# Performance work log

Hardware: AMD Instinct MI355X
Metric: run time of the kernel (lower is better)

Reference implementation:

```python
import jax, jax.numpy as jnp
import numpy as np

EPS = 1e-5
BN_GAMMA = 1.0
BN_BETA = 1e-4  # per torch init: BN weight=1, bias=0.0001


def bn(h):
    # BatchNorm1d in training mode: biased batch variance
    mu = h.mean(axis=0)
    var = h.var(axis=0)
    return (h - mu) * (BN_GAMMA / jnp.sqrt(var + EPS)) + BN_BETA


def gcn_conv(h, W, b, row, col, n, edge_weight=None):
    # PyG-style GCNConv: linear -> add self loops (w=1) -> sym deg norm -> scatter-sum
    h = h @ W
    e = row.shape[0]
    ew = jnp.ones((e,), h.dtype) if edge_weight is None else edge_weight
    loop = jnp.arange(n, dtype=row.dtype)
    r = jnp.concatenate([row, loop])
    c = jnp.concatenate([col, loop])
    w = jnp.concatenate([ew, jnp.ones((n,), h.dtype)])
    deg = jax.ops.segment_sum(w, r, num_segments=n)
    dinv = jnp.where(deg > 0, jax.lax.rsqrt(deg + jnp.where(deg > 0, 0.0, 1.0)), 0.0)
    norm = dinv[r] * w * dinv[c]  # [E+N]
    msg = h[r] * norm[:, None]    # gather + per-edge scale
    out = jax.ops.segment_sum(msg, c, num_segments=n)  # scatter-aggregate
    return out + b


def readout(h, W1, b1, W2, b2):
    h = bn(h) @ W1 + b1
    h = bn(jax.nn.relu(h)) @ W2 + b2
    return jax.nn.log_softmax(h, axis=-1)


def setup_inputs() -> dict:
    key = jax.random.key(0)
    ks = jax.random.split(key, 12)
    N, E, F, H, C = 50000, 800000, 128, 128, 10
    s = 0.05
    return {
        "x": jax.random.normal(ks[0], (N, F), jnp.float32),
        "edge_index": jax.random.randint(ks[1], (2, E), 0, N, jnp.int32),
        "perm": jax.random.permutation(ks[2], N).astype(jnp.int32),
        "W_feat": jax.random.normal(ks[3], (F, H), jnp.float32) * s,
        "b_feat": jnp.zeros((H,), jnp.float32),
        "W_convs": jax.random.normal(ks[4], (3, H, H), jnp.float32) * s,
        "b_convs": jnp.zeros((3, H), jnp.float32),
        "W_ea": jax.random.normal(ks[5], (2 * H, 2), jnp.float32) * s,
        "b_ea": jnp.zeros((2,), jnp.float32),
        "W_na": jax.random.normal(ks[6], (H, 2), jnp.float32) * s,
        "b_na": jnp.zeros((2,), jnp.float32),
        "W_ctx": jax.random.normal(ks[7], (H, H), jnp.float32) * s,
        "b_ctx": jnp.zeros((H,), jnp.float32),
        "W_obj": jax.random.normal(ks[8], (H, H), jnp.float32) * s,
        "b_obj": jnp.zeros((H,), jnp.float32),
        "W_fc1": jax.random.normal(ks[9], (3, H, H), jnp.float32) * s,  # c,o,co
        "b_fc1": jnp.zeros((3, H), jnp.float32),
        "W_fc2": jax.random.normal(ks[10], (3, H, C), jnp.float32) * s,
        "b_fc2": jnp.zeros((3, C), jnp.float32),
    }


def reference(x, edge_index, perm, W_feat, b_feat, W_convs, b_convs, W_ea, b_ea,
              W_na, b_na, W_ctx, b_ctx, W_obj, b_obj, W_fc1, b_fc1, W_fc2, b_fc2):
    n = x.shape[0]
    row, col = edge_index[0], edge_index[1]
    h = bn(x)
    h = jax.nn.relu(h @ W_feat + b_feat)  # conv_feat has gfn=True -> pure linear
    for i in range(3):
        h = jax.nn.relu(gcn_conv(bn(h), W_convs[i], b_convs[i], row, col, n))
    edge_rep = jnp.concatenate([h[row], h[col]], axis=-1)  # [E, 2H]
    edge_att = jax.nn.softmax(edge_rep @ W_ea + b_ea, axis=-1)
    node_att = jax.nn.softmax(h @ W_na + b_na, axis=-1)
    xc = node_att[:, 0:1] * h
    xo = node_att[:, 1:2] * h
    xc = jax.nn.relu(gcn_conv(bn(xc), W_ctx, b_ctx, row, col, n, edge_att[:, 0]))
    xo = jax.nn.relu(gcn_conv(bn(xo), W_obj, b_obj, row, col, n, edge_att[:, 1]))
    xc_logis = readout(xc, W_fc1[0], b_fc1[0], W_fc2[0], b_fc2[0])
    xo_logis = readout(xo, W_fc1[1], b_fc1[1], W_fc2[1], b_fc2[1])
    xco_logis = readout(xc[perm] + xo, W_fc1[2], b_fc1[2], W_fc2[2], b_fc2[2])
    return (xc_logis, xo_logis, xco_logis)
```

## Files before the change

### kernel.cpp

```cpp
#include <hip/hip_runtime.h>
#include <math.h>

#define H 128
#define NCLS 10
#define EPS 1e-5f
#define BN_BETA 1e-4f
#define CS_BLOCKS 256

typedef unsigned short u16;
typedef unsigned int u32;
typedef __attribute__((ext_vector_type(8))) short short8;
typedef __attribute__((ext_vector_type(4))) float floatx4;

__device__ inline float bflo(u32 u) { union { u32 i; float f; } a; a.i = u << 16; return a.f; }
__device__ inline float bfhi(u32 u) { union { u32 i; float f; } a; a.i = u & 0xffff0000u; return a.f; }
__device__ inline u16 f2bf(float f) {
  union { float f; u32 i; } v; v.f = f;
  return (u16)((v.i + 0x7fff + ((v.i >> 16) & 1)) >> 16);
}
__device__ inline u32 pack2(float a, float b) { return (u32)f2bf(a) | ((u32)f2bf(b) << 16); }

__device__ inline void reduce_partials(const float* __restrict__ P, int nb, int stride,
                                       int off0, int f, float* su_out, float* sq_out) {
  float su[8] = {0, 0, 0, 0, 0, 0, 0, 0}, sq[8] = {0, 0, 0, 0, 0, 0, 0, 0};
  int b = 0;
  for (; b + 8 <= nb; b += 8) {
#pragma unroll
    for (int u = 0; u < 8; u++) {
      const float* p = P + (size_t)(b + u) * stride + off0;
      su[u] += p[f];
      sq[u] += p[128 + f];
    }
  }
  for (; b < nb; b++) {
    const float* p = P + (size_t)b * stride + off0;
    su[0] += p[f];
    sq[0] += p[128 + f];
  }
  *su_out = ((su[0] + su[1]) + (su[2] + su[3])) + ((su[4] + su[5]) + (su[6] + su[7]));
  *sq_out = ((sq[0] + sq[1]) + (sq[2] + sq[3])) + ((sq[4] + sq[5]) + (sq[6] + sq[7]));
}

__device__ inline void fold256_body(const float* P, int nb, int stride, int off0,
                                    const float* W, const float* bias, float invN,
                                    int kp, u16* Wt, float* cf) {
  int f = threadIdx.x & 127;
  int half = threadIdx.x >> 7;
  int k = kp * 2 + half;
  float su, sq;
  reduce_partials(P, nb, stride, off0, f, &su, &sq);
  float mu = su * invN;
  float var = sq * invN - mu * mu;
  float s = 1.0f / sqrtf(fmaxf(var, 0.f) + EPS);
  float w = W[(size_t)f * H + k];
  Wt[(size_t)k * H + f] = f2bf(s * w);
  __shared__ float red[2][128];
  red[half][f] = (BN_BETA - mu * s) * w;
  __syncthreads();
  for (int o = 64; o > 0; o >>= 1) {
    if (f < o) red[half][f] += red[half][f + o];
    __syncthreads();
  }
  if (f == 0) cf[k] = red[half][0] + (bias ? bias[k] : 0.f);
}

__device__ inline void hist_body(const int* __restrict__ row, const int* __restrict__ col,
                                 int E, int* cnt_in, int* cnt_out,
                                 int* rank_in, int* rank_out, int blk) {
  int e = blk * 256 + threadIdx.x;
  if (e < E) {
    rank_in[e] = atomicAdd(&cnt_in[col[e]], 1);
    rank_out[e] = atomicAdd(&cnt_out[row[e]], 1);
  }
}

__device__ inline void xstats_body(const float* __restrict__ x, int n4,
                                   float* __restrict__ stp, int blk) {
  int tid = threadIdx.x;
  int lane = tid & 63, wave = tid >> 6;
  float s[4] = {0, 0, 0, 0}, q[4] = {0, 0, 0, 0};
  int step = CS_BLOCKS * 256;
  for (int i = blk * 256 + tid; i < n4; i += step) {
    float4 v = ((const float4*)x)[i];
    s[0] += v.x; q[0] += v.x * v.x; s[1] += v.y; q[1] += v.y * v.y;
    s[2] += v.z; q[2] += v.z * v.z; s[3] += v.w; q[3] += v.w * v.w;
  }
#pragma unroll
  for (int k = 0; k < 4; k++) { s[k] += __shfl_xor(s[k], 32); q[k] += __shfl_xor(q[k], 32); }
  __shared__ float smx[4][256];
  int col = (lane & 31) * 4;
  if (lane < 32) {
#pragma unroll
    for (int k = 0; k < 4; k++) { smx[wave][col + k] = s[k]; smx[wave][128 + col + k] = q[k]; }
  }
  __syncthreads();
  stp[(size_t)blk * 256 + tid] = smx[0][tid] + smx[1][tid] + smx[2][tid] + smx[3][tid];
}

__device__ inline void scanA_body(const int* cnt_in, const int* cnt_out, int N,
                                  int* partial_in, int* partial_out, float* dinv, int blk) {
  int i = blk * 256 + threadIdx.x;
  int vo = (i < N) ? cnt_out[i] : 0;
  if (i < N) dinv[i] = 1.0f / sqrtf((float)vo + 1.0f);
  __shared__ int sdA[256];
  sdA[threadIdx.x] = (i < N) ? cnt_in[i] : 0;
  __syncthreads();
  for (int o = 128; o > 0; o >>= 1) {
    if (threadIdx.x < o) sdA[threadIdx.x] += sdA[threadIdx.x + o];
    __syncthreads();
  }
  if (threadIdx.x == 0) partial_in[blk] = sdA[0];
  __syncthreads();
  sdA[threadIdx.x] = vo;
  __syncthreads();
  for (int o = 128; o > 0; o >>= 1) {
    if (threadIdx.x < o) sdA[threadIdx.x] += sdA[threadIdx.x + o];
    __syncthreads();
  }
  if (threadIdx.x == 0) partial_out[blk] = sdA[0];
}

__device__ inline void scanB1(const int* partial, int nb, int* blockoff) {
  __shared__ int sdB[256];
  int t = threadIdx.x;
  int v = (t < nb) ? partial[t] : 0;
  sdB[t] = v;
  __syncthreads();
  for (int o = 1; o < 256; o <<= 1) {
    int x = (t >= o) ? sdB[t - o] : 0;
    __syncthreads();
    sdB[t] += x;
    __syncthreads();
  }
  blockoff[t] = sdB[t] - v;
  __syncthreads();
}

__device__ inline void scanC1(const int* cnt, int N, const int* blockoff,
                              int* off, int E, int blk) {
  __shared__ int sdC[256];
  int t = threadIdx.x;
  int i = blk * 256 + t;
  int v = (i < N) ? cnt[i] : 0;
  sdC[t] = v;
  __syncthreads();
  for (int o = 1; o < 256; o <<= 1) {
    int x = (t >= o) ? sdC[t - o] : 0;
    __syncthreads();
    sdC[t] += x;
    __syncthreads();
  }
  if (i < N) off[i] = blockoff[blk] + sdC[t] - v;
  if (i == 0) off[N] = E;
  __syncthreads();
}

__device__ inline void place_body(const int* row, const int* col, int E,
                                  const int* rank_in, const int* rank_out,
                                  const int* off_in, const int* off_out,
                                  const float* dinv, int* csr_src, int* slot_in,
                                  int* sout, float* wn, int blk) {
  int e = blk * 256 + threadIdx.x;
  if (e < E) {
    int c = col[e], r = row[e];
    int si = off_in[c] + rank_in[e];
    csr_src[si] = r;
    slot_in[e] = si;
    wn[si] = dinv[r];
    sout[e] = off_out[r] + rank_out[e];
  }
}

__device__ inline void eatt_body(const int* row, const int* col, int E,
                                 const float2* p01, const float2* q01,
                                 const float* b_ea, const int* slot_in,
                                 const int* sout, float* att0s, float* att_r, int blk) {
  int e = blk * 256 + threadIdx.x;
  if (e >= E) return;
  int r = row[e], c = col[e];
  float2 p = p01[r], q = q01[c];
  float l0 = p.x + q.x + b_ea[0];
  float l1 = p.y + q.y + b_ea[1];
  float a0 = 1.0f / (1.0f + expf(l1 - l0));
  att0s[slot_in[e]] = a0;
  att_r[sout[e]] = a0;
}

__device__ inline void degsum_body(const float* att_r, const int* off_out,
                                   float* degc, int N, int blk) {
  int v = blk * 256 + threadIdx.x;
  if (v >= N) return;
  int s0 = off_out[v], s1 = off_out[v + 1];
  float s = 0.f;
  for (int i = s0; i < s1; i++) s += att_r[i];
  degc[v] = s;
}

__device__ inline void xprestats_body(const u16* __restrict__ h,
                                      const float2* __restrict__ na01, int n4,
                                      float* __restrict__ stp, int blk) {
  int tid = threadIdx.x;
  int lane = tid & 63, wave = tid >> 6;
  float sc[4] = {0, 0, 0, 0}, qc[4] = {0, 0, 0, 0};
  float so[4] = {0, 0, 0, 0}, qo[4] = {0, 0, 0, 0};
  int step = CS_BLOCKS * 256;
  for (int i = blk * 256 + tid; i < n4; i += step) {
    int n = i >> 5;
    uint2 u = ((const uint2*)h)[i];
    float v0 = bflo(u.x), v1 = bfhi(u.x), v2 = bflo(u.y), v3 = bfhi(u.y);
    float2 ab = na01[n];
    float a = ab.x, b = ab.y;
    float c0 = v0 * a, c1 = v1 * a, c2 = v2 * a, c3 = v3 * a;
    float o0 = v0 * b, o1 = v1 * b, o2 = v2 * b, o3 = v3 * b;
    sc[0] += c0; qc[0] += c0 * c0; sc[1] += c1; qc[1] += c1 * c1;
    sc[2] += c2; qc[2] += c2 * c2; sc[3] += c3; qc[3] += c3 * c3;
    so[0] += o0; qo[0] += o0 * o0; so[1] += o1; qo[1] += o1 * o1;
    so[2] += o2; qo[2] += o2 * o2; so[3] += o3; qo[3] += o3 * o3;
  }
#pragma unroll
  for (int k = 0; k < 4; k++) {
    sc[k] += __shfl_xor(sc[k], 32); qc[k] += __shfl_xor(qc[k], 32);
    so[k] += __shfl_xor(so[k], 32); qo[k] += __shfl_xor(qo[k], 32);
  }
  __shared__ float smp[4][512];
  int col = (lane & 31) * 4;
  if (lane < 32) {
#pragma unroll
    for (int k = 0; k < 4; k++) {
      smp[wave][col + k] = sc[k];
      smp[wave][128 + col + k] = qc[k];
      smp[wave][256 + col + k] = so[k];
      smp[wave][384 + col + k] = qo[k];
    }
  }
  __syncthreads();
  float r0 = smp[0][tid] + smp[1][tid] + smp[2][tid] + smp[3][tid];
  float r1 = smp[0][256 + tid] + smp[1][256 + tid] + smp[2][256 + tid] + smp[3][256 + tid];
  stp[(size_t)blk * 512 + tid] = r0;
  stp[(size_t)blk * 512 + 256 + tid] = r1;
}

__device__ inline void gemm_core(const u16* A, const float* Afp, const u16* Bt,
                                 const float* cf, const float* b2, const float* sumw,
                                 u16* C, int N, int relu, int blk, float* stp) {
  int tid = threadIdx.x;
  int wave = tid >> 6, lane = tid & 63;
  int l15 = lane & 15, quad = lane >> 4;
  int row0 = (blk * 4 + wave) * 16;
  if (row0 >= N && !stp) return;
  int arow = row0 + l15;
  short8 a[4];
  short8 z8 = {0, 0, 0, 0, 0, 0, 0, 0};
  if (Afp) {
#pragma unroll
    for (int k4 = 0; k4 < 4; k4++) {
      if (arow < N) {
        const float* p = Afp + (size_t)arow * H + k4 * 32 + quad * 8;
        float4 f0 = *(const float4*)p;
        float4 f1 = *(const float4*)(p + 4);
        union { short8 s8; u32 u[4]; } cv;
        cv.u[0] = pack2(f0.x, f0.y); cv.u[1] = pack2(f0.z, f0.w);
        cv.u[2] = pack2(f1.x, f1.y); cv.u[3] = pack2(f1.z, f1.w);
        a[k4] = cv.s8;
      } else a[k4] = z8;
    }
  } else {
#pragma unroll
    for (int k4 = 0; k4 < 4; k4++)
      a[k4] = (arow < N) ? *(const short8*)(A + (size_t)arow * H + k4 * 32 + quad * 8) : z8;
  }
  float srow[4];
  if (sumw) {
#pragma unroll
    for (int r = 0; r < 4; r++) {
      int row = row0 + quad * 4 + r;
      srow[r] = (row < N) ? sumw[row] : 0.f;
    }
  }
  float ps[8], pq[8];
#pragma unroll
  for (int nt = 0; nt < 8; nt++) {
    floatx4 acc = {0.f, 0.f, 0.f, 0.f};
    const u16* bp = Bt + (size_t)(nt * 16 + l15) * H + quad * 8;
#pragma unroll
    for (int k4 = 0; k4 < 4; k4++) {
      short8 b = *(const short8*)(bp + k4 * 32);
      acc = __builtin_amdgcn_mfma_f32_16x16x32_bf16(a[k4], b, acc, 0, 0, 0);
    }
    int col = nt * 16 + l15;
    float base = cf[col];
    float bb = b2 ? b2[col] : 0.f;
    float s_ = 0.f, q_ = 0.f;
#pragma unroll
    for (int r = 0; r < 4; r++) {
      int row = row0 + quad * 4 + r;
      if (row < N) {
        float v = acc[r] + (sumw ? srow[r] * base + bb : base);
        if (relu) v = fmaxf(v, 0.f);
        s_ += v; q_ += v * v;
        C[(size_t)row * H + col] = f2bf(v);
      }
    }
    ps[nt] = s_; pq[nt] = q_;
  }
  if (stp) {
    __shared__ float sred[4][256];
#pragma unroll
    for (int nt = 0; nt < 8; nt++) {
      ps[nt] += __shfl_xor(ps[nt], 16); ps[nt] += __shfl_xor(ps[nt], 32);
      pq[nt] += __shfl_xor(pq[nt], 16); pq[nt] += __shfl_xor(pq[nt], 32);
    }
    if (quad == 0) {
#pragma unroll
      for (int nt = 0; nt < 8; nt++) {
        sred[wave][nt * 16 + l15] = ps[nt];
        sred[wave][128 + nt * 16 + l15] = pq[nt];
      }
    }
    __syncthreads();
    stp[(size_t)blk * 256 + tid] =
        sred[0][tid] + sred[1][tid] + sred[2][tid] + sred[3][tid];
  }
}

__global__ __launch_bounds__(256) void hist_xstats_kernel(
    const int* row, const int* col, int E, int* cnt_in, int* cnt_out,
    int* rank_in, int* rank_out, int gE, const float* x, int n4, float* stpX) {
  if ((int)blockIdx.x < gE)
    hist_body(row, col, E, cnt_in, cnt_out, rank_in, rank_out, blockIdx.x);
  else
    xstats_body(x, n4, stpX, blockIdx.x - gE);
}

__global__ __launch_bounds__(256) void scanA_fold_kernel(
    const int* cnt_in, const int* cnt_out, int N, int* partial_in, int* partial_out,
    float* dinv, int SB, const float* stpX, const float* W_feat, const float* b_feat,
    float invN, u16* WtA, float* cfA) {
  if ((int)blockIdx.x < SB)
    scanA_body(cnt_in, cnt_out, N, partial_in, partial_out, dinv, blockIdx.x);
  else
    fold256_body(stpX, CS_BLOCKS, 256, 0, W_feat, b_feat, invN, blockIdx.x - SB, WtA, cfA);
}

__global__ __launch_bounds__(256) void scanB_gemmx_kernel(
    const int* partial_in, const int* partial_out, int nb, int* blockoff_in,
    int* blockoff_out, const float* x, const u16* WtA, const float* cfA, u16* C,
    int N, float* stpG) {
  if (blockIdx.x == 0) {
    scanB1(partial_in, nb, blockoff_in);
    scanB1(partial_out, nb, blockoff_out);
  } else {
    gemm_core(nullptr, x, WtA, cfA, nullptr, nullptr, C, N, 1, blockIdx.x - 1, stpG);
  }
}

__global__ __launch_bounds__(256) void scanC_fold_kernel(
    const int* cnt_in, const int* cnt_out, int N, const int* blockoff_in,
    const int* blockoff_out, int* off_in, int* off_out, int E, int SB,
    const float* stpG, int nbG, const float* Wc, float invN, u16* WtB, float* cfB) {
  if ((int)blockIdx.x < SB) {
    scanC1(cnt_in, N, blockoff_in, off_in, E, blockIdx.x);
    scanC1(cnt_out, N, blockoff_out, off_out, E, blockIdx.x);
  } else {
    fold256_body(stpG, nbG, 256, 0, Wc, nullptr, invN, blockIdx.x - SB, WtB, cfB);
  }
}

__global__ __launch_bounds__(256) void place_gemm_kernel(
    const int* row, const int* col, int E, const int* rank_in, const int* rank_out,
    const int* off_in, const int* off_out, const float* dinv, int* csr_src,
    int* slot_in, int* sout, float* wn, int gE,
    const u16* A, const u16* WtB, const float* cfB, u16* C, int N) {
  if ((int)blockIdx.x < gE)
    place_body(row, col, E, rank_in, rank_out, off_in, off_out, dinv, csr_src,
               slot_in, sout, wn, blockIdx.x);
  else
    gemm_core(A, nullptr, WtB, cfB, nullptr, nullptr, C, N, 0, blockIdx.x - gE, nullptr);
}

__global__ __launch_bounds__(256) void eatt_xpre_kernel(
    const int* row, const int* col, int E, const float2* p01, const float2* q01,
    const float* b_ea, const int* slot_in, const int* sout, float* att0s,
    float* att_r, int gE, const u16* h, const float2* na01, int n4, float* stpPre) {
  if ((int)blockIdx.x < gE)
    eatt_body(row, col, E, p01, q01, b_ea, slot_in, sout, att0s, att_r, blockIdx.x);
  else
    xprestats_body(h, na01, n4, stpPre, blockIdx.x - gE);
}

__global__ __launch_bounds__(256) void degsum_fold2_kernel(
    const float* att_r, const int* off_out, float* degc, int N, int gN,
    const float* stpPre, const float* W_ctx, const float* W_obj, float invN,
    u16* Wt2, float* cf2) {
  if ((int)blockIdx.x < gN)
    degsum_body(att_r, off_out, degc, N, blockIdx.x);
  else {
    int b = blockIdx.x - gN;
    int j = b >> 6, kp = b & 63;
    fold256_body(stpPre, CS_BLOCKS, 512, j * 256, j ? W_obj : W_ctx, nullptr, invN, kp,
                 Wt2 + (size_t)j * H * H, cf2 + j * H);
  }
}

__global__ __launch_bounds__(256) void permadd_fold31_kernel(
    const u16* xc, const u16* xo, const int* perm, u16* outb, int n4, float* stpCO,
    const float* stpG, int nbG, const float* W_fc1, const float* b_fc1, float invN,
    u16* Wt3, float* cf3) {
  int tid = threadIdx.x;
  if ((int)blockIdx.x >= CS_BLOCKS) {
    int b = blockIdx.x - CS_BLOCKS;
    int j = b >> 6, kp = b & 63;
    fold256_body(stpG + (size_t)j * nbG * 256, nbG, 256, 0, W_fc1 + (size_t)j * H * H,
                 b_fc1 + j * H, invN, kp, Wt3 + (size_t)j * H * H, cf3 + j * H);
    return;
  }
  int blk = blockIdx.x;
  int lane = tid & 63, wave = tid >> 6;
  float s[4] = {0, 0, 0, 0}, q[4] = {0, 0, 0, 0};
  int step = CS_BLOCKS * 256;
  for (int i = blk * 256 + tid; i < n4; i += step) {
    int n = i >> 5, k = i & 31;
    int p = perm[n];
    uint2 a = ((const uint2*)xc)[(size_t)p * 32 + k];
    uint2 b = ((const uint2*)xo)[i];
    float f0 = bflo(a.x) + bflo(b.x), f1 = bfhi(a.x) + bfhi(b.x);
    float f2 = bflo(a.y) + bflo(b.y), f3 = bfhi(a.y) + bfhi(b.y);
    ((uint2*)outb)[i] = make_uint2(pack2(f0, f1), pack2(f2, f3));
    s[0] += f0; q[0] += f0 * f0; s[1] += f1; q[1] += f1 * f1;
    s[2] += f2; q[2] += f2 * f2; s[3] += f3; q[3] += f3 * f3;
  }
#pragma unroll
  for (int k = 0; k < 4; k++) { s[k] += __shfl_xor(s[k], 32); q[k] += __shfl_xor(q[k], 32); }
  __shared__ float smq[4][256];
  int col = (lane & 31) * 4;
  if (lane < 32) {
#pragma unroll
    for (int k = 0; k < 4; k++) { smq[wave][col + k] = s[k]; smq[wave][128 + col + k] = q[k]; }
  }
  __syncthreads();
  stpCO[(size_t)blk * 256 + tid] = smq[0][tid] + smq[1][tid] + smq[2][tid] + smq[3][tid];
}

__global__ __launch_bounds__(256) void fold256_kernel(
    const float* P, int nb, const float* W, const float* bias, float invN,
    u16* Wt, float* cf) {
  fold256_body(P, nb, 256, 0, W, bias, invN, blockIdx.x, Wt, cf);
}

__global__ __launch_bounds__(128) void fold10x3_kernel(
    const float* stpZ, int nb, const float* W_fc2, const float* b_fc2, float invN,
    float* W2f, float* c2f) {
  int j = blockIdx.x / NCLS, k = blockIdx.x % NCLS;
  const float* P = stpZ + (size_t)j * nb * 256;
  int f = threadIdx.x;
  float su, sq;
  reduce_partials(P, nb, 256, 0, f, &su, &sq);
  float mu = su * invN;
  float var = sq * invN - mu * mu;
  float s = 1.0f / sqrtf(fmaxf(var, 0.f) + EPS);
  float w = W_fc2[(size_t)j * H * NCLS + (size_t)f * NCLS + k];
  W2f[(size_t)j * H * NCLS + (size_t)f * NCLS + k] = s * w;
  __shared__ float red1[H];
  red1[f] = (BN_BETA - mu * s) * w;
  __syncthreads();
  for (int o = 64; o > 0; o >>= 1) {
    if (f < o) red1[f] += red1[f + o];
    __syncthreads();
  }
  if (f == 0) c2f[j * 16 + k] = red1[0] + b_fc2[j * NCLS + k];
}

__global__ __launch_bounds__(256) void gemm_kernel(
    const u16* A, const u16* Bt, const float* cf, u16* C, int N, int relu) {
  gemm_core(A, nullptr, Bt, cf, nullptr, nullptr, C, N, relu, blockIdx.x, nullptr);
}

__global__ __launch_bounds__(256) void gemm2sw_kernel(
    u16* B0, u16* B1, const u16* Wt2, const float* cf2,
    const float* b0, const float* b1, const float* sw0, const float* sw1,
    int N, int gG, float* stp) {
  int j = blockIdx.x / gG, blk = blockIdx.x % gG;
  u16* Z = j ? B1 : B0;
  gemm_core(Z, nullptr, Wt2 + (size_t)j * H * H, cf2 + j * H, j ? b1 : b0,
            j ? sw1 : sw0, Z, N, 1, blk, stp + (size_t)j * gG * 256);
}

__global__ __launch_bounds__(256) void gemm3_kernel(
    u16* Z0, u16* Z1, u16* Z2, const u16* Wt3, const float* cf3,
    int N, int gG, float* stp) {
  int j = blockIdx.x / gG, blk = blockIdx.x % gG;
  u16* Z = (j == 0) ? Z0 : (j == 1) ? Z1 : Z2;
  gemm_core(Z, nullptr, Wt3 + (size_t)j * H * H, cf3 + j * H, nullptr, nullptr,
            Z, N, 1, blk, stp + (size_t)j * gG * 256);
}

__global__ __launch_bounds__(256) void colstats_kernel(
    const u16* __restrict__ X, int N, float* __restrict__ stp) {
  int tid = threadIdx.x;
  int li = tid & 15, rg = tid >> 4;
  int wave = tid >> 6, lane = tid & 63;
  const uint4* T = (const uint4*)X;
  float s[8] = {0, 0, 0, 0, 0, 0, 0, 0}, q[8] = {0, 0, 0, 0, 0, 0, 0, 0};
  for (int r = blockIdx.x * 16 + rg; r < N; r += CS_BLOCKS * 16) {
    uint4 u = T[(size_t)r * 16 + li];
    float f[8] = {bflo(u.x), bfhi(u.x), bflo(u.y), bfhi(u.y),
                  bflo(u.z), bfhi(u.z), bflo(u.w), bfhi(u.w)};
#pragma unroll
    for (int j = 0; j < 8; j++) { s[j] += f[j]; q[j] += f[j] * f[j]; }
  }
#pragma unroll
  for (int j = 0; j < 8; j++) {
    s[j] += __shfl_xor(s[j], 16); s[j] += __shfl_xor(s[j], 32);
    q[j] += __shfl_xor(q[j], 16); q[j] += __shfl_xor(q[j], 32);
  }
  __shared__ float smc[4][256];
  if ((lane & 48) == 0) {
#pragma unroll
    for (int j = 0; j < 8; j++) {
      smc[wave][li * 8 + j] = s[j];
      smc[wave][128 + li * 8 + j] = q[j];
    }
  }
  __syncthreads();
  stp[(size_t)blockIdx.x * 256 + tid] = smc[0][tid] + smc[1][tid] + smc[2][tid] + smc[3][tid];
}

#define ACC8(A, U, W)                                             \
  A[0] += (W) * bflo(U.x); A[1] += (W) * bfhi(U.x);               \
  A[2] += (W) * bflo(U.y); A[3] += (W) * bfhi(U.y);               \
  A[4] += (W) * bflo(U.z); A[5] += (W) * bfhi(U.z);               \
  A[6] += (W) * bflo(U.w); A[7] += (W) * bfhi(U.w);

__global__ __launch_bounds__(256) void agg_kernel(
    const u16* __restrict__ t, const int* __restrict__ csr_src,
    const float* __restrict__ wseg, const int* __restrict__ off,
    const float* __restrict__ dinv, const float* __restrict__ bias,
    u16* __restrict__ out, int N) {
  int v = blockIdx.x * 4 + (threadIdx.x >> 6);
  if (v >= N) return;
  int lane = threadIdx.x & 63;
  int g = lane >> 4, li = lane & 15;
  const uint4* T = (const uint4*)t;
  float dv = dinv[v];
  float acc[8] = {0.f, 0.f, 0.f, 0.f, 0.f, 0.f, 0.f, 0.f};
  if (g == 0) {
    uint4 u = T[(size_t)v * 16 + li];
    float w0 = dv * dv;
    ACC8(acc, u, w0)
  }
  int s0 = off[v], s1 = off[v + 1];
  for (int s = s0; s < s1; s += 32) {
    int ix[8]; float wv[8];
#pragma unroll
    for (int u = 0; u < 8; u++) {
      int e = s + g + u * 4;
      bool ok = e < s1;
      int e2 = ok ? e : s0;
      ix[u] = csr_src[e2];
      wv[u] = ok ? wseg[e2] : 0.f;
    }
    uint4 uu[8];
#pragma unroll
    for (int u = 0; u < 8; u++) uu[u] = T[(size_t)ix[u] * 16 + li];
#pragma unroll
    for (int u = 0; u < 8; u++) { float w = wv[u] * dv; ACC8(acc, uu[u], w) }
  }
#pragma unroll
  for (int j = 0; j < 8; j++) {
    acc[j] += __shfl_xor(acc[j], 16);
    acc[j] += __shfl_xor(acc[j], 32);
  }
  if (g == 0) {
    float o[8];
#pragma unroll
    for (int j = 0; j < 8; j++) o[j] = fmaxf(acc[j] + bias[li * 8 + j], 0.f);
    uint4 w4;
    w4.x = pack2(o[0], o[1]); w4.y = pack2(o[2], o[3]);
    w4.z = pack2(o[4], o[5]); w4.w = pack2(o[6], o[7]);
    ((uint4*)out)[(size_t)v * 16 + li] = w4;
  }
}

__global__ __launch_bounds__(256) void aggdual_kernel(
    const u16* __restrict__ h, const int* __restrict__ csr_src,
    const float* __restrict__ att0s, const int* __restrict__ cnt_out,
    const float* __restrict__ degc, const float2* __restrict__ na01,
    const int* __restrict__ off,
    u16* __restrict__ gc, u16* __restrict__ go,
    float* __restrict__ sumw_c, float* __restrict__ sumw_o, int N) {
  int v = blockIdx.x * 4 + (threadIdx.x >> 6);
  if (v >= N) return;
  int lane = threadIdx.x & 63;
  int g = lane >> 4, li = lane & 15;
  const uint4* T = (const uint4*)h;
  float dgc = degc[v];
  float dvc = 1.0f / sqrtf(dgc + 1.0f);
  float dvo = 1.0f / sqrtf((float)cnt_out[v] - dgc + 1.0f);
  float ac[8] = {0.f, 0.f, 0.f, 0.f, 0.f, 0.f, 0.f, 0.f};
  float ao[8] = {0.f, 0.f, 0.f, 0.f, 0.f, 0.f, 0.f, 0.f};
  float swc = 0.f, swo = 0.f;
  if (g == 0) {
    uint4 u = T[(size_t)v * 16 + li];
    float2 na = na01[v];
    float wc = dvc * dvc, wo = dvo * dvo;
    float wch = wc * na.x, woh = wo * na.y;
    ACC8(ac, u, wch)
    ACC8(ao, u, woh)
  }
  int s0 = off[v], s1 = off[v + 1];
  for (int s = s0; s < s1; s += 16) {
    int ix[4]; float a0v[4];
#pragma unroll
    for (int u = 0; u < 4; u++) {
      int e = s + g + u * 4;
      bool ok = e < s1;
      int e2 = ok ? e : s0;
      ix[u] = csr_src[e2];
      a0v[u] = ok ? att0s[e2] : 0.f;
      if (!ok) a0v[u] = -1.f;
    }
    uint4 uu[4];
    float2 nav[4];
    float dS[4], dC[4];
#pragma unroll
    for (int u = 0; u < 4; u++) {
      int sidx = ix[u];
      uu[u] = T[(size_t)sidx * 16 + li];
      nav[u] = na01[sidx];
      dS[u] = (float)cnt_out[sidx];
      dC[u] = degc[sidx];
    }
#pragma unroll
    for (int u = 0; u < 4; u++) {
      float a0 = a0v[u];
      bool ok = a0 >= 0.f;
      float r0 = ok ? a0 / sqrtf(dC[u] + 1.0f) : 0.f;
      float r1 = ok ? (1.0f - a0) / sqrtf(dS[u] - dC[u] + 1.0f) : 0.f;
      float wc = r0 * nav[u].x * dvc; ACC8(ac, uu[u], wc)
      float wo = r1 * nav[u].y * dvo; ACC8(ao, uu[u], wo)
      swc += r0; swo += r1;
    }
  }
#pragma unroll
  for (int j = 0; j < 8; j++) {
    ac[j] += __shfl_xor(ac[j], 16); ac[j] += __shfl_xor(ac[j], 32);
    ao[j] += __shfl_xor(ao[j], 16); ao[j] += __shfl_xor(ao[j], 32);
  }
  swc += __shfl_xor(swc, 16); swc += __shfl_xor(swc, 32);
  swo += __shfl_xor(swo, 16); swo += __shfl_xor(swo, 32);
  if (g == 0) {
    uint4 wc4, wo4;
    wc4.x = pack2(ac[0], ac[1]); wc4.y = pack2(ac[2], ac[3]);
    wc4.z = pack2(ac[4], ac[5]); wc4.w = pack2(ac[6], ac[7]);
    wo4.x = pack2(ao[0], ao[1]); wo4.y = pack2(ao[2], ao[3]);
    wo4.z = pack2(ao[4], ao[5]); wo4.w = pack2(ao[6], ao[7]);
    ((uint4*)gc)[(size_t)v * 16 + li] = wc4;
    ((uint4*)go)[(size_t)v * 16 + li] = wo4;
    if (li == 0) {
      sumw_c[v] = dvc * swc + dvc * dvc;
      sumw_o[v] = dvo * swo + dvo * dvo;
    }
  }
}

__global__ __launch_bounds__(256) void natt_kernel(
    const u16* __restrict__ h, int N,
    const float* __restrict__ W_na, const float* __restrict__ b_na,
    const float* __restrict__ W_ea,
    float2* __restrict__ na01, float2* __restrict__ p01, float2* __restrict__ q01) {
  int n = blockIdx.x * 256 + threadIdx.x;
  if (n >= N) return;
  float sa0 = 0, sa1 = 0, sp0 = 0, sp1 = 0, sq0 = 0, sq1 = 0;
  const uint2* hr = (const uint2*)(h + (size_t)n * H);
  for (int c = 0; c < 32; c++) {
    uint2 u = hr[c];
    float v0 = bflo(u.x), v1 = bfhi(u.x), v2 = bflo(u.y), v3 = bfhi(u.y);
    int k = c * 4;
    sa0 += v0 * W_na[k * 2] + v1 * W_na[k * 2 + 2] + v2 * W_na[k * 2 + 4] + v3 * W_na[k * 2 + 6];
    sa1 += v0 * W_na[k * 2 + 1] + v1 * W_na[k * 2 + 3] + v2 * W_na[k * 2 + 5] + v3 * W_na[k * 2 + 7];
    sp0 += v0 * W_ea[k * 2] + v1 * W_ea[k * 2 + 2] + v2 * W_ea[k * 2 + 4] + v3 * W_ea[k * 2 + 6];
    sp1 += v0 * W_ea[k * 2 + 1] + v1 * W_ea[k * 2 + 3] + v2 * W_ea[k * 2 + 5] + v3 * W_ea[k * 2 + 7];
    sq0 += v0 * W_ea[(H + k) * 2] + v1 * W_ea[(H + k) * 2 + 2] + v2 * W_ea[(H + k) * 2 + 4] + v3 * W_ea[(H + k) * 2 + 6];
    sq1 += v0 * W_ea[(H + k) * 2 + 1] + v1 * W_ea[(H + k) * 2 + 3] + v2 * W_ea[(H + k) * 2 + 5] + v3 * W_ea[(H + k) * 2 + 7];
  }
  sa0 += b_na[0]; sa1 += b_na[1];
  float m = fmaxf(sa0, sa1);
  float e0 = expf(sa0 - m), e1 = expf(sa1 - m);
  float inv = 1.f / (e0 + e1);
  na01[n] = make_float2(e0 * inv, e1 * inv);
  p01[n] = make_float2(sp0, sp1);
  q01[n] = make_float2(sq0, sq1);
}

__global__ __launch_bounds__(256) void fc2x3_kernel(
    const u16* __restrict__ z0, const u16* __restrict__ z1, const u16* __restrict__ z2,
    const float* __restrict__ W2f, const float* __restrict__ c2f,
    float* __restrict__ outp, int N, int gN) {
  int j = blockIdx.x / gN, blk = blockIdx.x % gN;
  int n = blk * 256 + threadIdx.x;
  if (n >= N) return;
  const u16* z = (j == 0) ? z0 : (j == 1) ? z1 : z2;
  const float* W2 = W2f + (size_t)j * H * NCLS;
  const float* c2 = c2f + j * 16;
  float* op = outp + (size_t)j * N * NCLS;
  float acc[NCLS];
#pragma unroll
  for (int c = 0; c < NCLS; c++) acc[c] = c2[c];
  const uint2* zr = (const uint2*)(z + (size_t)n * H);
  for (int c4 = 0; c4 < 32; c4++) {
    uint2 u = zr[c4];
    float v[4] = {bflo(u.x), bfhi(u.x), bflo(u.y), bfhi(u.y)};
    int k = c4 * 4;
#pragma unroll
    for (int jj = 0; jj < 4; jj++)
#pragma unroll
      for (int c = 0; c < NCLS; c++) acc[c] += v[jj] * W2[(k + jj) * NCLS + c];
  }
  float m = acc[0];
#pragma unroll
  for (int c = 1; c < NCLS; c++) m = fmaxf(m, acc[c]);
  float s = 0.f;
#pragma unroll
  for (int c = 0; c < NCLS; c++) s += expf(acc[c] - m);
  float lse = logf(s) + m;
#pragma unroll
  for (int c = 0; c < NCLS; c++) op[(size_t)n * NCLS + c] = acc[c] - lse;
}

extern "C" void kernel_launch(void* const* d_in, const int* in_sizes, int n_in,
                              void* d_out, int out_size, void* d_ws, size_t ws_size,
                              hipStream_t stream) {
  const int N = in_sizes[0] / H;
  const int E = in_sizes[1] / 2;
  const float* x = (const float*)d_in[0];
  const int* ei = (const int*)d_in[1];
  const int* row = ei;
  const int* col = ei + E;
  const int* perm = (const int*)d_in[2];
  const float* W_feat = (const float*)d_in[3];
  const float* b_feat = (const float*)d_in[4];
  const float* W_convs = (const float*)d_in[5];
  const float* b_convs = (const float*)d_in[6];
  const float* W_ea = (const float*)d_in[7];
  const float* b_ea = (const float*)d_in[8];
  const float* W_na = (const float*)d_in[9];
  const float* b_na = (const float*)d_in[10];
  const float* W_ctx = (const float*)d_in[11];
  const float* b_ctx = (const float*)d_in[12];
  const float* W_obj = (const float*)d_in[13];
  const float* b_obj = (const float*)d_in[14];
  const float* W_fc1 = (const float*)d_in[15];
  const float* b_fc1 = (const float*)d_in[16];
  const float* W_fc2 = (const float*)d_in[17];
  const float* b_fc2 = (const float*)d_in[18];
  float* out = (float*)d_out;

  const int gG = (N + 63) / 64;
  const int gN = (N + 255) / 256;
  const int gE = (E + 255) / 256;
  const int SB = (N + 255) / 256;
  const int n4 = N * 32;
  const int gAgg = (N + 3) / 4;
  const float invN = 1.0f / (float)N;

  char* base = (char*)d_ws;
  size_t off_b = 0;
  auto alloc = [&](size_t bytes) -> void* {
    void* p = base + off_b;
    off_b = (off_b + bytes + 255) & ~(size_t)255;
    return p;
  };
  size_t NB2 = (size_t)N * H * sizeof(u16);
  u16* bufA = (u16*)alloc(NB2);
  u16* bufB = (u16*)alloc(NB2);
  u16* bufC = (u16*)alloc(NB2);
  u16* bufD = (u16*)alloc(NB2);
  int* cnt_in = (int*)alloc(2 * (size_t)N * 4);
  int* cnt_out = cnt_in + N;
  float* degc = (float*)alloc((size_t)N * 4);
  float* stpX = (float*)alloc((size_t)CS_BLOCKS * 256 * 4);
  float* stpG = (float*)alloc(3 * (size_t)gG * 256 * 4);
  float* stpPre = (float*)alloc((size_t)CS_BLOCKS * 512 * 4);
  float* stpCO = (float*)alloc((size_t)CS_BLOCKS * 256 * 4);
  int* off_in = (int*)alloc(((size_t)N + 1) * 4);
  int* off_out = (int*)alloc(((size_t)N + 1) * 4);
  float* dinv = (float*)alloc((size_t)N * 4);
  float* sumw_c = (float*)alloc((size_t)N * 4);
  float* sumw_o = (float*)alloc((size_t)N * 4);
  float2* na01 = (float2*)alloc((size_t)N * 8);
  float2* p01 = (float2*)alloc((size_t)N * 8);
  float2* q01 = (float2*)alloc((size_t)N * 8);
  int* partial_in = (int*)alloc(256 * 4);
  int* partial_out = (int*)alloc(256 * 4);
  int* blockoff_in = (int*)alloc(256 * 4);
  int* blockoff_out = (int*)alloc(256 * 4);
  u16* WtA = (u16*)alloc((size_t)H * H * 2);
  u16* WtB = (u16*)alloc((size_t)H * H * 2);
  u16* Wt2 = (u16*)alloc(2 * (size_t)H * H * 2);
  u16* Wt3 = (u16*)alloc(3 * (size_t)H * H * 2);
  float* cfA = (float*)alloc(H * 4);
  float* cfB = (float*)alloc(H * 4);
  float* cf2 = (float*)alloc(2 * H * 4);
  float* cf3 = (float*)alloc(3 * H * 4);
  float* W2f = (float*)alloc(3 * (size_t)H * NCLS * 4);
  float* c2f = (float*)alloc(3 * 16 * 4);
  int* rank_in = (int*)alloc((size_t)E * 4);
  int* rank_out = (int*)alloc((size_t)E * 4);
  int* csr_src = (int*)alloc((size_t)E * 4);
  int* slot_in = (int*)alloc((size_t)E * 4);
  int* sout = (int*)alloc((size_t)E * 4);
  float* att0s = (float*)alloc((size_t)E * 4);
  float* att_r = (float*)alloc((size_t)E * 4);
  float* wn = (float*)alloc((size_t)E * 4);

  hipMemsetAsync(cnt_in, 0, 2 * (size_t)N * 4, stream);

  hist_xstats_kernel<<<gE + CS_BLOCKS, 256, 0, stream>>>(
      row, col, E, cnt_in, cnt_out, rank_in, rank_out, gE, x, n4, stpX);
  scanA_fold_kernel<<<SB + 64, 256, 0, stream>>>(
      cnt_in, cnt_out, N, partial_in, partial_out, dinv, SB, stpX, W_feat, b_feat,
      invN, WtA, cfA);
  scanB_gemmx_kernel<<<1 + gG, 256, 0, stream>>>(
      partial_in, partial_out, SB, blockoff_in, blockoff_out, x, WtA, cfA, bufA, N, stpG);
  scanC_fold_kernel<<<SB + 64, 256, 0, stream>>>(
      cnt_in, cnt_out, N, blockoff_in, blockoff_out, off_in, off_out, E, SB,
      stpG, gG, W_convs, invN, WtB, cfB);
  place_gemm_kernel<<<gE + gG, 256, 0, stream>>>(
      row, col, E, rank_in, rank_out, off_in, off_out, dinv, csr_src, slot_in, sout,
      wn, gE, bufA, WtB, cfB, bufB, N);
  agg_kernel<<<gAgg, 256, 0, stream>>>(bufB, csr_src, wn, off_in, dinv, b_convs, bufA, N);

  for (int i = 1; i < 3; ++i) {
    colstats_kernel<<<CS_BLOCKS, 256, 0, stream>>>(bufA, N, stpX);
    fold256_kernel<<<64, 256, 0, stream>>>(stpX, CS_BLOCKS, W_convs + (size_t)i * H * H,
                                           nullptr, invN, WtB, cfB);
    gemm_kernel<<<gG, 256, 0, stream>>>(bufA, WtB, cfB, bufB, N, 0);
    agg_kernel<<<gAgg, 256, 0, stream>>>(bufB, csr_src, wn, off_in, dinv,
                                         b_convs + (size_t)i * H, bufA, N);
  }

  natt_kernel<<<gN, 256, 0, stream>>>(bufA, N, W_na, b_na, W_ea, na01, p01, q01);
  eatt_xpre_kernel<<<gE + CS_BLOCKS, 256, 0, stream>>>(
      row, col, E, p01, q01, b_ea, slot_in, sout, att0s, att_r, gE,
      bufA, na01, n4, stpPre);
  degsum_fold2_kernel<<<gN + 128, 256, 0, stream>>>(
      att_r, off_out, degc, N, gN, stpPre, W_ctx, W_obj, invN, Wt2, cf2);
  aggdual_kernel<<<gAgg, 256, 0, stream>>>(bufA, csr_src, att0s, cnt_out, degc, na01,
                                           off_in, bufC, bufD, sumw_c, sumw_o, N);
  gemm2sw_kernel<<<2 * gG, 256, 0, stream>>>(bufC, bufD, Wt2, cf2, b_ctx, b_obj,
                                             sumw_c, sumw_o, N, gG, stpG);

  permadd_fold31_kernel<<<CS_BLOCKS + 128, 256, 0, stream>>>(
      bufC, bufD, perm, bufA, n4, stpCO, stpG, gG, W_fc1, b_fc1, invN, Wt3, cf3);
  fold256_kernel<<<64, 256, 0, stream>>>(stpCO, CS_BLOCKS, W_fc1 + 2 * (size_t)H * H,
                                         b_fc1 + 2 * H, invN, Wt3 + 2 * (size_t)H * H,
                                         cf3 + 2 * H);
  gemm3_kernel<<<3 * gG, 256, 0, stream>>>(bufC, bufD, bufA, Wt3, cf3, N, gG, stpG);
  fold10x3_kernel<<<3 * NCLS, 128, 0, stream>>>(stpG, gG, W_fc2, b_fc2, invN, W2f, c2f);
  fc2x3_kernel<<<3 * gN, 256, 0, stream>>>(bufC, bufD, bufA, W2f, c2f, out, N, gN);
}
```

Baseline: 833.2 us.

## Fuse node-attention projection into last GCN aggregation and pack per-node attention factors

Fuses the node/edge attention projections into the final GCN aggregation kernel, so the freshly computed rows feed the dot products directly and the separate natt pass, which re-read all of h, is removed. The two-class edge softmax is rewritten as a sigmoid of a precomputed per-node logit difference, so each edge gathers one float from each endpoint instead of two float2 values. The degree sum now also precomputes per-node inverse square-root degrees and their products with node attention into a float4, so the dual aggregation does one 16-byte gather per source instead of three gathers plus two square roots. The cost is extra shuffle reductions in the aggregation kernel and a new N×16-byte buffer.

```diff
diff --git a/kernel.cpp b/kernel.cpp
--- a/kernel.cpp
+++ b/kernel.cpp
@@ -172,28 +172,27 @@
 }
 
 __device__ inline void eatt_body(const int* row, const int* col, int E,
-                                 const float2* p01, const float2* q01,
-                                 const float* b_ea, const int* slot_in,
-                                 const int* sout, float* att0s, float* att_r, int blk) {
+                                 const float* dp, const float* dq,
+                                 const int* slot_in, const int* sout,
+                                 float* att0s, float* att_r, int blk) {
   int e = blk * 256 + threadIdx.x;
   if (e >= E) return;
-  int r = row[e], c = col[e];
-  float2 p = p01[r], q = q01[c];
-  float l0 = p.x + q.x + b_ea[0];
-  float l1 = p.y + q.y + b_ea[1];
-  float a0 = 1.0f / (1.0f + expf(l1 - l0));
+  float a0 = 1.0f / (1.0f + expf(-(dp[row[e]] + dq[col[e]])));
   att0s[slot_in[e]] = a0;
   att_r[sout[e]] = a0;
 }
 
-__device__ inline void degsum_body(const float* att_r, const int* off_out,
-                                   float* degc, int N, int blk) {
+__device__ inline void degsum_f4_body(const float* att_r, const int* off_out,
+                                      const float2* na01, float4* f4, int N, int blk) {
   int v = blk * 256 + threadIdx.x;
   if (v >= N) return;
   int s0 = off_out[v], s1 = off_out[v + 1];
   float s = 0.f;
   for (int i = s0; i < s1; i++) s += att_r[i];
-  degc[v] = s;
+  float dvc = 1.0f / sqrtf(s + 1.0f);
+  float dvo = 1.0f / sqrtf((float)(s1 - s0) - s + 1.0f);
+  float2 na = na01[v];
+  f4[v] = make_float4(dvc, dvo, dvc * na.x, dvo * na.y);
 }
 
 __device__ inline void xprestats_body(const u16* __restrict__ h,
@@ -379,21 +378,22 @@
 }
 
 __global__ __launch_bounds__(256) void eatt_xpre_kernel(
-    const int* row, const int* col, int E, const float2* p01, const float2* q01,
-    const float* b_ea, const int* slot_in, const int* sout, float* att0s,
+    const int* row, const int* col, int E, const float* dp, const float* dq,
+    const int* slot_in, const int* sout, float* att0s,
     float* att_r, int gE, const u16* h, const float2* na01, int n4, float* stpPre) {
   if ((int)blockIdx.x < gE)
-    eatt_body(row, col, E, p01, q01, b_ea, slot_in, sout, att0s, att_r, blockIdx.x);
+    eatt_body(row, col, E, dp, dq, slot_in, sout, att0s, att_r, blockIdx.x);
   else
     xprestats_body(h, na01, n4, stpPre, blockIdx.x - gE);
 }
 
 __global__ __launch_bounds__(256) void degsum_fold2_kernel(
-    const float* att_r, const int* off_out, float* degc, int N, int gN,
+    const float* att_r, const int* off_out, const float2* na01, float4* f4,
+    int N, int gN,
     const float* stpPre, const float* W_ctx, const float* W_obj, float invN,
     u16* Wt2, float* cf2) {
   if ((int)blockIdx.x < gN)
-    degsum_body(att_r, off_out, degc, N, blockIdx.x);
+    degsum_f4_body(att_r, off_out, na01, f4, N, blockIdx.x);
   else {
     int b = blockIdx.x - gN;
     int j = b >> 6, kp = b & 63;
@@ -581,10 +581,86 @@
   }
 }
 
+__global__ __launch_bounds__(256) void agg_natt_kernel(
+    const u16* __restrict__ t, const int* __restrict__ csr_src,
+    const float* __restrict__ wseg, const int* __restrict__ off,
+    const float* __restrict__ dinv, const float* __restrict__ bias,
+    const float* __restrict__ W_na, const float* __restrict__ b_na,
+    const float* __restrict__ W_ea, const float* __restrict__ b_ea,
+    u16* __restrict__ out, float2* __restrict__ na01,
+    float* __restrict__ dp, float* __restrict__ dq, int N) {
+  int v = blockIdx.x * 4 + (threadIdx.x >> 6);
+  if (v >= N) return;
+  int lane = threadIdx.x & 63;
+  int g = lane >> 4, li = lane & 15;
+  const uint4* T = (const uint4*)t;
+  float dv = dinv[v];
+  float acc[8] = {0.f, 0.f, 0.f, 0.f, 0.f, 0.f, 0.f, 0.f};
+  if (g == 0) {
+    uint4 u = T[(size_t)v * 16 + li];
+    float w0 = dv * dv;
+    ACC8(acc, u, w0)
+  }
+  int s0 = off[v], s1 = off[v + 1];
+  for (int s = s0; s < s1; s += 32) {
+    int ix[8]; float wv[8];
+#pragma unroll
+    for (int u = 0; u < 8; u++) {
+      int e = s + g + u * 4;
+      bool ok = e < s1;
+      int e2 = ok ? e : s0;
+      ix[u] = csr_src[e2];
+      wv[u] = ok ? wseg[e2] : 0.f;
+    }
+    uint4 uu[8];
+#pragma unroll
+    for (int u = 0; u < 8; u++) uu[u] = T[(size_t)ix[u] * 16 + li];
+#pragma unroll
+    for (int u = 0; u < 8; u++) { float w = wv[u] * dv; ACC8(acc, uu[u], w) }
+  }
+#pragma unroll
+  for (int j = 0; j < 8; j++) {
+    acc[j] += __shfl_xor(acc[j], 16);
+    acc[j] += __shfl_xor(acc[j], 32);
+  }
+  float o[8];
+#pragma unroll
+  for (int j = 0; j < 8; j++) o[j] = fmaxf(acc[j] + bias[li * 8 + j], 0.f);
+  if (g == 0) {
+    uint4 w4;
+    w4.x = pack2(o[0], o[1]); w4.y = pack2(o[2], o[3]);
+    w4.z = pack2(o[4], o[5]); w4.w = pack2(o[6], o[7]);
+    ((uint4*)out)[(size_t)v * 16 + li] = w4;
+  }
+  float d0 = 0, d1 = 0, d2 = 0, d3 = 0, d4 = 0, d5 = 0;
+#pragma unroll
+  for (int j = 0; j < 8; j++) {
+    int k = li * 8 + j;
+    float hv = o[j];
+    d0 += hv * W_na[k * 2];       d1 += hv * W_na[k * 2 + 1];
+    d2 += hv * W_ea[k * 2];       d3 += hv * W_ea[k * 2 + 1];
+    d4 += hv * W_ea[(H + k) * 2]; d5 += hv * W_ea[(H + k) * 2 + 1];
+  }
+#pragma unroll
+  for (int m = 1; m < 16; m <<= 1) {
+    d0 += __shfl_xor(d0, m); d1 += __shfl_xor(d1, m);
+    d2 += __shfl_xor(d2, m); d3 += __shfl_xor(d3, m);
+    d4 += __shfl_xor(d4, m); d5 += __shfl_xor(d5, m);
+  }
+  if (g == 0 && li == 0) {
+    float sa0 = d0 + b_na[0], sa1 = d1 + b_na[1];
+    float mm = fmaxf(sa0, sa1);
+    float e0 = expf(sa0 - mm), e1 = expf(sa1 - mm);
+    float inv = 1.f / (e0 + e1);
+    na01[v] = make_float2(e0 * inv, e1 * inv);
+    dp[v] = (d2 + b_ea[0]) - (d3 + b_ea[1]);
+    dq[v] = d4 - d5;
+  }
+}
+
 __global__ __launch_bounds__(256) void aggdual_kernel(
     const u16* __restrict__ h, const int* __restrict__ csr_src,
-    const float* __restrict__ att0s, const int* __restrict__ cnt_out,
-    const float* __restrict__ degc, const float2* __restrict__ na01,
+    const float* __restrict__ att0s, const float4* __restrict__ f4,
     const int* __restrict__ off,
     u16* __restrict__ gc, u16* __restrict__ go,
     float* __restrict__ sumw_c, float* __restrict__ sumw_o, int N) {
@@ -593,17 +669,14 @@
   int lane = threadIdx.x & 63;
   int g = lane >> 4, li = lane & 15;
   const uint4* T = (const uint4*)h;
-  float dgc = degc[v];
-  float dvc = 1.0f / sqrtf(dgc + 1.0f);
-  float dvo = 1.0f / sqrtf((float)cnt_out[v] - dgc + 1.0f);
+  float4 fv = f4[v];
+  float dvc = fv.x, dvo = fv.y;
   float ac[8] = {0.f, 0.f, 0.f, 0.f, 0.f, 0.f, 0.f, 0.f};
   float ao[8] = {0.f, 0.f, 0.f, 0.f, 0.f, 0.f, 0.f, 0.f};
   float swc = 0.f, swo = 0.f;
   if (g == 0) {
     uint4 u = T[(size_t)v * 16 + li];
-    float2 na = na01[v];
-    float wc = dvc * dvc, wo = dvo * dvo;
-    float wch = wc * na.x, woh = wo * na.y;
+    float wch = dvc * fv.z, woh = dvo * fv.w;
     ACC8(ac, u, wch)
     ACC8(ao, u, woh)
   }
@@ -616,29 +689,25 @@
       bool ok = e < s1;
       int e2 = ok ? e : s0;
       ix[u] = csr_src[e2];
-      a0v[u] = ok ? att0s[e2] : 0.f;
-      if (!ok) a0v[u] = -1.f;
+      a0v[u] = ok ? att0s[e2] : -1.f;
     }
     uint4 uu[4];
-    float2 nav[4];
-    float dS[4], dC[4];
+    float4 fs[4];
 #pragma unroll
     for (int u = 0; u < 4; u++) {
       int sidx = ix[u];
       uu[u] = T[(size_t)sidx * 16 + li];
-      nav[u] = na01[sidx];
-      dS[u] = (float)cnt_out[sidx];
-      dC[u] = degc[sidx];
+      fs[u] = f4[sidx];
     }
 #pragma unroll
     for (int u = 0; u < 4; u++) {
       float a0 = a0v[u];
       bool ok = a0 >= 0.f;
-      float r0 = ok ? a0 / sqrtf(dC[u] + 1.0f) : 0.f;
-      float r1 = ok ? (1.0f - a0) / sqrtf(dS[u] - dC[u] + 1.0f) : 0.f;
-      float wc = r0 * nav[u].x * dvc; ACC8(ac, uu[u], wc)
-      float wo = r1 * nav[u].y * dvo; ACC8(ao, uu[u], wo)
-      swc += r0; swo += r1;
+      float a1 = ok ? (1.0f - a0) : 0.f;
+      if (!ok) a0 = 0.f;
+      float wc = a0 * fs[u].z * dvc; ACC8(ac, uu[u], wc)
+      float wo = a1 * fs[u].w * dvo; ACC8(ao, uu[u], wo)
+      swc += a0 * fs[u].x; swo += a1 * fs[u].y;
     }
   }
 #pragma unroll
@@ -661,35 +730,6 @@
       sumw_o[v] = dvo * swo + dvo * dvo;
     }
   }
-}
-
-__global__ __launch_bounds__(256) void natt_kernel(
-    const u16* __restrict__ h, int N,
-    const float* __restrict__ W_na, const float* __restrict__ b_na,
-    const float* __restrict__ W_ea,
-    float2* __restrict__ na01, float2* __restrict__ p01, float2* __restrict__ q01) {
-  int n = blockIdx.x * 256 + threadIdx.x;
-  if (n >= N) return;
-  float sa0 = 0, sa1 = 0, sp0 = 0, sp1 = 0, sq0 = 0, sq1 = 0;
-  const uint2* hr = (const uint2*)(h + (size_t)n * H);
-  for (int c = 0; c < 32; c++) {
-    uint2 u = hr[c];
-    float v0 = bflo(u.x), v1 = bfhi(u.x), v2 = bflo(u.y), v3 = bfhi(u.y);
-    int k = c * 4;
-    sa0 += v0 * W_na[k * 2] + v1 * W_na[k * 2 + 2] + v2 * W_na[k * 2 + 4] + v3 * W_na[k * 2 + 6];
-    sa1 += v0 * W_na[k * 2 + 1] + v1 * W_na[k * 2 + 3] + v2 * W_na[k * 2 + 5] + v3 * W_na[k * 2 + 7];
-    sp0 += v0 * W_ea[k * 2] + v1 * W_ea[k * 2 + 2] + v2 * W_ea[k * 2 + 4] + v3 * W_ea[k * 2 + 6];
-    sp1 += v0 * W_ea[k * 2 + 1] + v1 * W_ea[k * 2 + 3] + v2 * W_ea[k * 2 + 5] + v3 * W_ea[k * 2 + 7];
-    sq0 += v0 * W_ea[(H + k) * 2] + v1 * W_ea[(H + k) * 2 + 2] + v2 * W_ea[(H + k) * 2 + 4] + v3 * W_ea[(H + k) * 2 + 6];
-    sq1 += v0 * W_ea[(H + k) * 2 + 1] + v1 * W_ea[(H + k) * 2 + 3] + v2 * W_ea[(H + k) * 2 + 5] + v3 * W_ea[(H + k) * 2 + 7];
-  }
-  sa0 += b_na[0]; sa1 += b_na[1];
-  float m = fmaxf(sa0, sa1);
-  float e0 = expf(sa0 - m), e1 = expf(sa1 - m);
-  float inv = 1.f / (e0 + e1);
-  na01[n] = make_float2(e0 * inv, e1 * inv);
-  p01[n] = make_float2(sp0, sp1);
-  q01[n] = make_float2(sq0, sq1);
 }
 
 __global__ __launch_bounds__(256) void fc2x3_kernel(
@@ -777,7 +817,6 @@
   u16* bufD = (u16*)alloc(NB2);
   int* cnt_in = (int*)alloc(2 * (size_t)N * 4);
   int* cnt_out = cnt_in + N;
-  float* degc = (float*)alloc((size_t)N * 4);
   float* stpX = (float*)alloc((size_t)CS_BLOCKS * 256 * 4);
   float* stpG = (float*)alloc(3 * (size_t)gG * 256 * 4);
   float* stpPre = (float*)alloc((size_t)CS_BLOCKS * 512 * 4);
@@ -788,8 +827,9 @@
   float* sumw_c = (float*)alloc((size_t)N * 4);
   float* sumw_o = (float*)alloc((size_t)N * 4);
   float2* na01 = (float2*)alloc((size_t)N * 8);
-  float2* p01 = (float2*)alloc((size_t)N * 8);
-  float2* q01 = (float2*)alloc((size_t)N * 8);
+  float* dp = (float*)alloc((size_t)N * 4);
+  float* dq = (float*)alloc((size_t)N * 4);
+  float4* f4 = (float4*)alloc((size_t)N * 16);
   int* partial_in = (int*)alloc(256 * 4);
   int* partial_out = (int*)alloc(256 * 4);
   int* blockoff_in = (int*)alloc(256 * 4);
@@ -830,22 +870,27 @@
       wn, gE, bufA, WtB, cfB, bufB, N);
   agg_kernel<<<gAgg, 256, 0, stream>>>(bufB, csr_src, wn, off_in, dinv, b_convs, bufA, N);
 
-  for (int i = 1; i < 3; ++i) {
-    colstats_kernel<<<CS_BLOCKS, 256, 0, stream>>>(bufA, N, stpX);
-    fold256_kernel<<<64, 256, 0, stream>>>(stpX, CS_BLOCKS, W_convs + (size_t)i * H * H,
-                                           nullptr, invN, WtB, cfB);
-    gemm_kernel<<<gG, 256, 0, stream>>>(bufA, WtB, cfB, bufB, N, 0);
-    agg_kernel<<<gAgg, 256, 0, stream>>>(bufB, csr_src, wn, off_in, dinv,
-                                         b_convs + (size_t)i * H, bufA, N);
-  }
-
-  natt_kernel<<<gN, 256, 0, stream>>>(bufA, N, W_na, b_na, W_ea, na01, p01, q01);
+  colstats_kernel<<<CS_BLOCKS, 256, 0, stream>>>(bufA, N, stpX);
+  fold256_kernel<<<64, 256, 0, stream>>>(stpX, CS_BLOCKS, W_convs + (size_t)1 * H * H,
+                                         nullptr, invN, WtB, cfB);
+  gemm_kernel<<<gG, 256, 0, stream>>>(bufA, WtB, cfB, bufB, N, 0);
+  agg_kernel<<<gAgg, 256, 0, stream>>>(bufB, csr_src, wn, off_in, dinv,
+                                       b_convs + (size_t)1 * H, bufA, N);
+
+  colstats_kernel<<<CS_BLOCKS, 256, 0, stream>>>(bufA, N, stpX);
+  fold256_kernel<<<64, 256, 0, stream>>>(stpX, CS_BLOCKS, W_convs + (size_t)2 * H * H,
+                                         nullptr, invN, WtB, cfB);
+  gemm_kernel<<<gG, 256, 0, stream>>>(bufA, WtB, cfB, bufB, N, 0);
+  agg_natt_kernel<<<gAgg, 256, 0, stream>>>(bufB, csr_src, wn, off_in, dinv,
+                                            b_convs + (size_t)2 * H, W_na, b_na,
+                                            W_ea, b_ea, bufA, na01, dp, dq, N);
+
   eatt_xpre_kernel<<<gE + CS_BLOCKS, 256, 0, stream>>>(
-      row, col, E, p01, q01, b_ea, slot_in, sout, att0s, att_r, gE,
+      row, col, E, dp, dq, slot_in, sout, att0s, att_r, gE,
       bufA, na01, n4, stpPre);
   degsum_fold2_kernel<<<gN + 128, 256, 0, stream>>>(
-      att_r, off_out, degc, N, gN, stpPre, W_ctx, W_obj, invN, Wt2, cf2);
-  aggdual_kernel<<<gAgg, 256, 0, stream>>>(bufA, csr_src, att0s, cnt_out, degc, na01,
+      att_r, off_out, na01, f4, N, gN, stpPre, W_ctx, W_obj, invN, Wt2, cf2);
+  aggdual_kernel<<<gAgg, 256, 0, stream>>>(bufA, csr_src, att0s, f4,
                                            off_in, bufC, bufD, sumw_c, sumw_o, N);
   gemm2sw_kernel<<<2 * gG, 256, 0, stream>>>(bufC, bufD, Wt2, cf2, b_ctx, b_obj,
                                              sumw_c, sumw_o, N, gG, stpG);
```

After: 841.7 us. About the same (+1.0%).
